# Optimization experiments

Hardware: AMD Instinct MI355X
Metric: run time of the kernel (lower is better)

The kernel has to match this reference:

```python
import jax
import jax.numpy as jnp
import numpy as np

NPOINT = 512
RADIUS = 0.2
K = 32


def setup_inputs() -> dict:
    key = jax.random.key(0)
    k1, k2 = jax.random.split(key)
    xyz = jax.random.uniform(k1, (8, 16384, 3), dtype=jnp.float32)      # [B,N,3] in unit cube
    features = jax.random.normal(k2, (8, 128, 16384), dtype=jnp.float32)  # [B,D,N]
    return {"xyz": xyz, "features": features}


def farthest_point_sample(xyz, npoint):
    # xyz: [B,N,3] -> centroids [B,npoint] int32. Deterministic start at index 0
    # (the torch code does randint(...)*0).
    B, N, _ = xyz.shape
    init_dist = jnp.full((B, N), 1e10, dtype=xyz.dtype)
    init_far = jnp.zeros((B,), dtype=jnp.int32)

    def step(carry, _):
        distance, farthest = carry
        centroid = jnp.take_along_axis(xyz, farthest[:, None, None], axis=1)  # [B,1,3]
        d = jnp.sum((xyz - centroid) ** 2, axis=-1)                           # [B,N]
        distance = jnp.minimum(distance, d)
        new_far = jnp.argmax(distance, axis=-1).astype(jnp.int32)
        return (distance, new_far), farthest

    (_, _), cents = jax.lax.scan(step, (init_dist, init_far), None, length=npoint)
    return cents.T  # [B, npoint]


def square_distance(src, dst):
    # src [B,S,3], dst [B,N,3] -> [B,S,N]
    d = -2.0 * jnp.einsum("bsc,bnc->bsn", src, dst)
    d = d + jnp.sum(src ** 2, -1)[:, :, None]
    d = d + jnp.sum(dst ** 2, -1)[:, None, :]
    return d


def query_ball_point(radius, nsample, xyz, new_xyz):
    B, N, _ = xyz.shape
    sqrd = square_distance(new_xyz, xyz)                              # [B,S,N]
    arangeN = jnp.arange(N, dtype=jnp.int32)[None, None, :]
    idx = jnp.where(sqrd > radius ** 2, N, arangeN)                   # out-of-ball -> sentinel N
    idx = jnp.sort(idx, axis=-1)[:, :, :nsample]                      # [B,S,K]
    first = idx[:, :, :1]
    idx = jnp.where(idx == N, first, idx)                             # pad with first valid neighbor
    return idx


def index_points(points, idx):
    # points [B,N,C], idx [B,...] -> [B,...,C]
    B = points.shape[0]
    bidx = jnp.arange(B).reshape((B,) + (1,) * (idx.ndim - 1))
    return points[bidx, idx]


def reference(xyz, features):
    # xyz [B,N,3], features [B,D,N]
    cent = farthest_point_sample(xyz, NPOINT)                 # [B,S]
    new_xyz = index_points(xyz, cent)                         # [B,S,3]
    idx = query_ball_point(RADIUS, K, xyz, new_xyz)           # [B,S,K]
    pts = jnp.transpose(features, (0, 2, 1))                  # [B,N,D]
    grouped = index_points(pts, idx)                          # [B,S,K,D]
    sub_features = jnp.max(grouped, axis=2)                   # [B,S,D]  (max over K neighbors)
    sub_features = jnp.transpose(sub_features, (0, 2, 1))     # [B,D,S]
    return new_xyz, sub_features
```

## Files before the change

kernel.cpp:

```cpp
#include <hip/hip_runtime.h>
#include <stdint.h>
#include <math.h>

#define NB      8
#define NPTS    16384
#define NPOINT  512
#define NCH     128
#define KNBR    32
#define R2      0.04f

#define FPS_THR 512
#define PPT     32

#define CENT_OFF 0
#define MAP_OFF  16384
#define FT_OFF   (16384 + 524288)

#define DPP_ARG_STEP(v, p, CTRL) do {                                          \
    float _ov = __builtin_bit_cast(float, __builtin_amdgcn_update_dpp(         \
        __builtin_bit_cast(int, (v)), __builtin_bit_cast(int, (v)),            \
        (CTRL), 0xF, 0xF, false));                                             \
    int _op = __builtin_amdgcn_update_dpp((p), (p), (CTRL), 0xF, 0xF, false);  \
    bool _t = (_ov > (v)) || ((_ov == (v)) && (_op < (p)));                    \
    (v) = _t ? _ov : (v);                                                      \
    (p) = _t ? _op : (p);                                                      \
} while (0)

__device__ __forceinline__ int cell_of(float x, float y, float z) {
    int cx = (int)(x * 8.0f); cx = cx < 0 ? 0 : (cx > 7 ? 7 : cx);
    int cy = (int)(y * 8.0f); cy = cy < 0 ? 0 : (cy > 7 ? 7 : cy);
    int cz = (int)(z * 8.0f); cz = cz < 0 ? 0 : (cz > 7 ? 7 : cz);
    int m = 0;
    m |= ((cx & 1) << 2) | ((cx & 2) << 4) | ((cx & 4) << 6);
    m |= ((cy & 1) << 1) | ((cy & 2) << 3) | ((cy & 4) << 5);
    m |=  (cz & 1)       | ((cz & 2) << 2) | ((cz & 4) << 4);
    return m;
}

__global__
__attribute__((amdgpu_flat_work_group_size(FPS_THR, FPS_THR)))
__attribute__((amdgpu_waves_per_eu(2, 2)))
void fps_transpose_kernel(const float* __restrict__ xyz,
                          const float* __restrict__ feat,
                          float* __restrict__ out,
                          int* __restrict__ cent,
                          int* __restrict__ map,
                          float* __restrict__ ft,
                          int use_ft)
{
    const int blk = blockIdx.x;
    const int tid = threadIdx.x;

    if (blk < NB) {
        const int b = blk;
        const float* xb = xyz + (size_t)b * NPTS * 3;
        int* gmap = map + b * NPTS;
        const int lane = tid & 63;
        const int wid  = tid >> 6;

        __shared__ int   s_hist[512];
        __shared__ float s_meta[8][PPT][4];
        __shared__ float s_v[2][8];
        __shared__ int   s_p[2][8];

        s_hist[tid] = 0;
        __syncthreads();
        for (int k = 0; k < PPT; ++k) {
            int p = k * FPS_THR + tid;
            int c = cell_of(xb[p * 3 + 0], xb[p * 3 + 1], xb[p * 3 + 2]);
            atomicAdd(&s_hist[c], 1);
        }
        __syncthreads();
        int mycount = s_hist[tid];
        for (int off = 1; off < 512; off <<= 1) {
            int v = (tid >= off) ? s_hist[tid - off] : 0;
            __syncthreads();
            s_hist[tid] += v;
            __syncthreads();
        }
        int excl = s_hist[tid] - mycount;
        __syncthreads();
        s_hist[tid] = excl;
        __syncthreads();
        for (int k = 0; k < PPT; ++k) {
            int p = k * FPS_THR + tid;
            int c = cell_of(xb[p * 3 + 0], xb[p * 3 + 1], xb[p * 3 + 2]);
            int pos = atomicAdd(&s_hist[c], 1);
            gmap[pos] = p;
        }
        __threadfence_block();
        __syncthreads();
        float px[PPT], py[PPT], pz[PPT], d[PPT];
        int   idx[PPT];
#pragma unroll
        for (int k = 0; k < PPT; ++k) {
            int pos = (k * 8 + wid) * 64 + lane;
            int op  = gmap[pos];
            idx[k] = op;
            px[k] = xb[op * 3 + 0];
            py[k] = xb[op * 3 + 1];
            pz[k] = xb[op * 3 + 2];
            d[k]  = 1e10f;
        }
#pragma unroll
        for (int k = 0; k < PPT; ++k) {
            float mnx = px[k], mxx = px[k];
            float mny = py[k], mxy = py[k];
            float mnz = pz[k], mxz = pz[k];
#pragma unroll
            for (int s = 1; s < 64; s <<= 1) {
                mnx = fminf(mnx, __shfl_xor(mnx, s, 64));
                mxx = fmaxf(mxx, __shfl_xor(mxx, s, 64));
                mny = fminf(mny, __shfl_xor(mny, s, 64));
                mxy = fmaxf(mxy, __shfl_xor(mxy, s, 64));
                mnz = fminf(mnz, __shfl_xor(mnz, s, 64));
                mxz = fmaxf(mxz, __shfl_xor(mxz, s, 64));
            }
            if (lane == 0) {
                float hx = (mxx - mnx) * 0.5f;
                float hy = (mxy - mny) * 0.5f;
                float hz = (mxz - mnz) * 0.5f;
                s_meta[wid][k][0] = (mnx + mxx) * 0.5f;
                s_meta[wid][k][1] = (mny + mxy) * 0.5f;
                s_meta[wid][k][2] = (mnz + mxz) * 0.5f;
                s_meta[wid][k][3] =
                    sqrtf(hx * hx + hy * hy + hz * hz) * 1.0001f + 1e-6f;
            }
        }
        __syncthreads();
        const float bmx = s_meta[wid][lane & 31][0];
        const float bmy = s_meta[wid][lane & 31][1];
        const float bmz = s_meta[wid][lane & 31][2];
        const float br  = s_meta[wid][lane & 31][3];
        float U = 1e10f;

        float cx = xb[0], cy = xb[1], cz = xb[2];
        if (tid == 0) {
            cent[b * NPOINT + 0] = 0;
            out[((size_t)b * NPOINT + 0) * 3 + 0] = cx;
            out[((size_t)b * NPOINT + 0) * 3 + 1] = cy;
            out[((size_t)b * NPOINT + 0) * 3 + 2] = cz;
        }

        for (int i = 1; i < NPOINT; ++i) {
            float dcx = cx - bmx, dcy = cy - bmy, dcz = cz - bmz;
            float dc  = sqrtf(dcx * dcx + dcy * dcy + dcz * dcz);
            float t   = dc - br;
            bool skip = (t > 0.0f) && (t * t >= U + 2e-5f);
            unsigned mask = (unsigned)__ballot(skip);

            if (mask != 0xFFFFFFFFu) {
#pragma unroll
                for (int k = 0; k < PPT; ++k) {
                    if (!(mask & (1u << k))) {
                        float dx = __fsub_rn(px[k], cx);
                        float dy = __fsub_rn(py[k], cy);
                        float dz = __fsub_rn(pz[k], cz);
                        float dd = __fadd_rn(__fadd_rn(__fmul_rn(dx, dx),
                                                       __fmul_rn(dy, dy)),
                                             __fmul_rn(dz, dz));
                        d[k] = fminf(d[k], dd);
                    }
                }
            }
            if (!((mask >> (lane & 31)) & 1u)) {
                float ub = dc + br;
                U = fminf(U, ub * ub * 1.0001f + 1e-6f);
            }
            float vmax = d[0];
#pragma unroll
            for (int k = 1; k < PPT; ++k) vmax = fmaxf(vmax, d[k]);
            int bi = idx[PPT - 1];
#pragma unroll
            for (int k = PPT - 2; k >= 0; --k) bi = (d[k] == vmax) ? idx[k] : bi;

            float rv = vmax;
            int   rp = bi;
            DPP_ARG_STEP(rv, rp, 0xB1);
            DPP_ARG_STEP(rv, rp, 0x4E);
            DPP_ARG_STEP(rv, rp, 0x141);
            DPP_ARG_STEP(rv, rp, 0x140);
            DPP_ARG_STEP(rv, rp, 0x142);
            DPP_ARG_STEP(rv, rp, 0x143);
            const int par = i & 1;
            if (lane == 63) { s_v[par][wid] = rv; s_p[par][wid] = rp; }
            __syncthreads();
            float fv = s_v[par][lane & 7];
            int   fp = s_p[par][lane & 7];
            DPP_ARG_STEP(fv, fp, 0xB1);
            DPP_ARG_STEP(fv, fp, 0x4E);
            DPP_ARG_STEP(fv, fp, 0x141);
            const int cur = __builtin_amdgcn_readfirstlane(fp);
            cx = xb[cur * 3 + 0];
            cy = xb[cur * 3 + 1];
            cz = xb[cur * 3 + 2];
            if (tid == 0) {
                cent[b * NPOINT + i] = cur;
                size_t o = ((size_t)b * NPOINT + i) * 3;
                out[o + 0] = cx; out[o + 1] = cy; out[o + 2] = cz;
            }
        }
    } else {
        if (!use_ft) return;
        int t  = blk - NB;
        int b  = t >> 11;
        int r  = t & 2047;
        int ct = r >> 9;
        int nt = r & 511;
        __shared__ float tile[32][33];
        int tx = tid & 31, ty = tid >> 5;
        tile[ty][tx] =
            feat[((size_t)b * NCH + ct * 32 + ty) * NPTS + nt * 32 + tx];
        tile[ty + 16][tx] =
            feat[((size_t)b * NCH + ct * 32 + ty + 16) * NPTS + nt * 32 + tx];
        __syncthreads();
        ft[((size_t)b * NPTS + nt * 32 + ty) * NCH + ct * 32 + tx] =
            tile[tx][ty];
        ft[((size_t)b * NPTS + nt * 32 + ty + 16) * NCH + ct * 32 + tx] =
            tile[tx][ty + 16];
    }
}

__global__ __launch_bounds__(256, 4)
void query_pool_kernel(const float* __restrict__ xyz,
                       const float* __restrict__ feat,
                       const float* __restrict__ ft,
                       const int* __restrict__ cent,
                       float* __restrict__ out_sub,
                       int use_ft)
{
    const int tid  = threadIdx.x;
    const int widx = tid >> 6;
    const int lane = tid & 63;
    const int w = blockIdx.x * 4 + widx;
    const int b = w >> 9;
    const int s = w & 511;

    const float* xb = xyz + (size_t)b * NPTS * 3;
    const int ci = cent[b * NPOINT + s];
    const float sx = xb[ci * 3 + 0];
    const float sy = xb[ci * 3 + 1];
    const float sz = xb[ci * 3 + 2];
    const float snorm = __fadd_rn(__fadd_rn(__fmul_rn(sx, sx),
                                            __fmul_rn(sy, sy)),
                                  __fmul_rn(sz, sz));

    __shared__ int lidx[4][KNBR];
    int found = 0;
    for (int base = 0; base < NPTS && found < KNBR; base += 64) {
        int j = base + lane;
        float dx = xb[j * 3 + 0];
        float dy = xb[j * 3 + 1];
        float dz = xb[j * 3 + 2];
        float dn = __fadd_rn(__fadd_rn(__fmul_rn(dx, dx),
                                       __fmul_rn(dy, dy)),
                             __fmul_rn(dz, dz));
        float dot = __fadd_rn(__fadd_rn(__fmul_rn(sx, dx),
                                        __fmul_rn(sy, dy)),
                              __fmul_rn(sz, dz));
        float d = __fadd_rn(__fadd_rn(__fmul_rn(-2.0f, dot), snorm), dn);
        bool inball = !(d > R2);
        unsigned long long mask = __ballot(inball);
        int before = (int)__popcll(mask & ((1ULL << lane) - 1ULL));
        int slot = found + before;
        if (inball && slot < KNBR) lidx[widx][slot] = j;
        found += (int)__popcll(mask);
    }
    int cnt = found < KNBR ? found : KNBR;
    __syncthreads();

    float a0 = -INFINITY, a1 = -INFINITY;
    if (use_ft) {
        for (int m = 0; m < cnt; ++m) {
            int i = lidx[widx][m];
            const float* row = ft + ((size_t)b * NPTS + i) * NCH;
            a0 = fmaxf(a0, row[lane]);
            a1 = fmaxf(a1, row[lane + 64]);
        }
    } else {
        for (int m = 0; m < cnt; ++m) {
            int i = lidx[widx][m];
            a0 = fmaxf(a0, feat[((size_t)b * NCH + lane) * NPTS + i]);
            a1 = fmaxf(a1, feat[((size_t)b * NCH + lane + 64) * NPTS + i]);
        }
    }
    out_sub[((size_t)b * NCH + lane) * NPOINT + s] = a0;
    out_sub[((size_t)b * NCH + lane + 64) * NPOINT + s] = a1;
}

extern "C" void kernel_launch(void* const* d_in, const int* in_sizes, int n_in,
                              void* d_out, int out_size, void* d_ws, size_t ws_size,
                              hipStream_t stream)
{
    const float* xyz  = (const float*)d_in[0];
    const float* feat = (const float*)d_in[1];
    float* out = (float*)d_out;

    int*   cent = (int*)((char*)d_ws + CENT_OFF);
    int*   map  = (int*)((char*)d_ws + MAP_OFF);
    float* ft   = (float*)((char*)d_ws + FT_OFF);
    const size_t need_ft = (size_t)FT_OFF + (size_t)NB * NPTS * NCH * 4ull;
    int use_ft = (ws_size >= need_ft) ? 1 : 0;

    int nblocks1 = NB + (use_ft ? NB * (NCH / 32) * (NPTS / 32) : 0);
    hipLaunchKernelGGL(fps_transpose_kernel, dim3(nblocks1), dim3(FPS_THR), 0, stream,
                       xyz, feat, out, cent, map, ft, use_ft);

    hipLaunchKernelGGL(query_pool_kernel, dim3((NB * NPOINT) / 4), dim3(256), 0, stream,
                       xyz, feat, ft, cent, out + (size_t)NB * NPOINT * 3, use_ft);
}
```

Baseline: 1.019 ms.

## Fuse FPS and ball-query pooling into one kernel with spin-wait on centroids

Measured after the change: 1.037 ms. About the same (+1.7%).

```diff
diff --git a/kernel.cpp b/kernel.cpp
--- a/kernel.cpp
+++ b/kernel.cpp
@@ -11,10 +11,10 @@
 
 #define FPS_THR 512
 #define PPT     32
+#define QBLKS   512
 
 #define CENT_OFF 0
 #define MAP_OFF  16384
-#define FT_OFF   (16384 + 524288)
 
 #define DPP_ARG_STEP(v, p, CTRL) do {                                          \
     float _ov = __builtin_bit_cast(float, __builtin_amdgcn_update_dpp(         \
@@ -39,24 +39,23 @@
 
 __global__
 __attribute__((amdgpu_flat_work_group_size(FPS_THR, FPS_THR)))
-__attribute__((amdgpu_waves_per_eu(2, 2)))
-void fps_transpose_kernel(const float* __restrict__ xyz,
-                          const float* __restrict__ feat,
-                          float* __restrict__ out,
-                          int* __restrict__ cent,
-                          int* __restrict__ map,
-                          float* __restrict__ ft,
-                          int use_ft)
+__attribute__((amdgpu_waves_per_eu(2, 4)))
+void fps_query_kernel(const float* __restrict__ xyz,
+                      const float* __restrict__ feat,
+                      float* __restrict__ out,
+                      int* __restrict__ cent,
+                      int* __restrict__ map,
+                      float* __restrict__ out_sub)
 {
     const int blk = blockIdx.x;
     const int tid = threadIdx.x;
+    const int lane = tid & 63;
+    const int wid  = tid >> 6;
 
     if (blk < NB) {
         const int b = blk;
         const float* xb = xyz + (size_t)b * NPTS * 3;
         int* gmap = map + b * NPTS;
-        const int lane = tid & 63;
-        const int wid  = tid >> 6;
 
         __shared__ int   s_hist[512];
         __shared__ float s_meta[8][PPT][4];
@@ -136,10 +135,11 @@
 
         float cx = xb[0], cy = xb[1], cz = xb[2];
         if (tid == 0) {
-            cent[b * NPOINT + 0] = 0;
             out[((size_t)b * NPOINT + 0) * 3 + 0] = cx;
             out[((size_t)b * NPOINT + 0) * 3 + 1] = cy;
             out[((size_t)b * NPOINT + 0) * 3 + 2] = cz;
+            __hip_atomic_store(&cent[b * NPOINT + 0], 0,
+                               __ATOMIC_RELAXED, __HIP_MEMORY_SCOPE_AGENT);
         }
 
         for (int i = 1; i < NPOINT; ++i) {
@@ -195,97 +195,66 @@
             cy = xb[cur * 3 + 1];
             cz = xb[cur * 3 + 2];
             if (tid == 0) {
-                cent[b * NPOINT + i] = cur;
                 size_t o = ((size_t)b * NPOINT + i) * 3;
                 out[o + 0] = cx; out[o + 1] = cy; out[o + 2] = cz;
+                __hip_atomic_store(&cent[b * NPOINT + i], cur,
+                                   __ATOMIC_RELAXED, __HIP_MEMORY_SCOPE_AGENT);
             }
         }
     } else {
-        if (!use_ft) return;
-        int t  = blk - NB;
-        int b  = t >> 11;
-        int r  = t & 2047;
-        int ct = r >> 9;
-        int nt = r & 511;
-        __shared__ float tile[32][33];
-        int tx = tid & 31, ty = tid >> 5;
-        tile[ty][tx] =
-            feat[((size_t)b * NCH + ct * 32 + ty) * NPTS + nt * 32 + tx];
-        tile[ty + 16][tx] =
-            feat[((size_t)b * NCH + ct * 32 + ty + 16) * NPTS + nt * 32 + tx];
-        __syncthreads();
-        ft[((size_t)b * NPTS + nt * 32 + ty) * NCH + ct * 32 + tx] =
-            tile[tx][ty];
-        ft[((size_t)b * NPTS + nt * 32 + ty + 16) * NCH + ct * 32 + tx] =
-            tile[tx][ty + 16];
+        __shared__ int lidx[8][KNBR];
+        const int wv = (blk - NB) * 8 + wid;
+        const int b  = wv >> 9;
+        const int s  = wv & 511;
+        const float* xb = xyz + (size_t)b * NPTS * 3;
+
+        int ci;
+        for (;;) {
+            ci = __hip_atomic_load(&cent[b * NPOINT + s],
+                                   __ATOMIC_RELAXED, __HIP_MEMORY_SCOPE_AGENT);
+            if (ci >= 0) break;
+            __builtin_amdgcn_s_sleep(8);
+        }
+
+        const float sx = xb[ci * 3 + 0];
+        const float sy = xb[ci * 3 + 1];
+        const float sz = xb[ci * 3 + 2];
+        const float snorm = __fadd_rn(__fadd_rn(__fmul_rn(sx, sx),
+                                                __fmul_rn(sy, sy)),
+                                      __fmul_rn(sz, sz));
+
+        int found = 0;
+        for (int base = 0; base < NPTS && found < KNBR; base += 64) {
+            int j = base + lane;
+            float dx = xb[j * 3 + 0];
+            float dy = xb[j * 3 + 1];
+            float dz = xb[j * 3 + 2];
+            float dn = __fadd_rn(__fadd_rn(__fmul_rn(dx, dx),
+                                           __fmul_rn(dy, dy)),
+                                 __fmul_rn(dz, dz));
+            float dot = __fadd_rn(__fadd_rn(__fmul_rn(sx, dx),
+                                            __fmul_rn(sy, dy)),
+                                  __fmul_rn(sz, dz));
+            float dqp = __fadd_rn(__fadd_rn(__fmul_rn(-2.0f, dot), snorm), dn);
+            bool inball = !(dqp > R2);
+            unsigned long long m = __ballot(inball);
+            int before = (int)__popcll(m & ((1ULL << lane) - 1ULL));
+            int slot = found + before;
+            if (inball && slot < KNBR) lidx[wid][slot] = j;
+            found += (int)__popcll(m);
+        }
+        int cnt = found < KNBR ? found : KNBR;
+
+        float a0 = -INFINITY, a1 = -INFINITY;
+        const float* fb = feat + (size_t)b * NCH * NPTS;
+        for (int m = 0; m < cnt; ++m) {
+            int i = lidx[wid][m];
+            a0 = fmaxf(a0, fb[(size_t)lane * NPTS + i]);
+            a1 = fmaxf(a1, fb[(size_t)(lane + 64) * NPTS + i]);
+        }
+        out_sub[((size_t)b * NCH + lane) * NPOINT + s] = a0;
+        out_sub[((size_t)b * NCH + lane + 64) * NPOINT + s] = a1;
     }
-}
-
-__global__ __launch_bounds__(256, 4)
-void query_pool_kernel(const float* __restrict__ xyz,
-                       const float* __restrict__ feat,
-                       const float* __restrict__ ft,
-                       const int* __restrict__ cent,
-                       float* __restrict__ out_sub,
-                       int use_ft)
-{
-    const int tid  = threadIdx.x;
-    const int widx = tid >> 6;
-    const int lane = tid & 63;
-    const int w = blockIdx.x * 4 + widx;
-    const int b = w >> 9;
-    const int s = w & 511;
-
-    const float* xb = xyz + (size_t)b * NPTS * 3;
-    const int ci = cent[b * NPOINT + s];
-    const float sx = xb[ci * 3 + 0];
-    const float sy = xb[ci * 3 + 1];
-    const float sz = xb[ci * 3 + 2];
-    const float snorm = __fadd_rn(__fadd_rn(__fmul_rn(sx, sx),
-                                            __fmul_rn(sy, sy)),
-                                  __fmul_rn(sz, sz));
-
-    __shared__ int lidx[4][KNBR];
-    int found = 0;
-    for (int base = 0; base < NPTS && found < KNBR; base += 64) {
-        int j = base + lane;
-        float dx = xb[j * 3 + 0];
-        float dy = xb[j * 3 + 1];
-        float dz = xb[j * 3 + 2];
-        float dn = __fadd_rn(__fadd_rn(__fmul_rn(dx, dx),
-                                       __fmul_rn(dy, dy)),
-                             __fmul_rn(dz, dz));
-        float dot = __fadd_rn(__fadd_rn(__fmul_rn(sx, dx),
-                                        __fmul_rn(sy, dy)),
-                              __fmul_rn(sz, dz));
-        float d = __fadd_rn(__fadd_rn(__fmul_rn(-2.0f, dot), snorm), dn);
-        bool inball = !(d > R2);
-        unsigned long long mask = __ballot(inball);
-        int before = (int)__popcll(mask & ((1ULL << lane) - 1ULL));
-        int slot = found + before;
-        if (inball && slot < KNBR) lidx[widx][slot] = j;
-        found += (int)__popcll(mask);
-    }
-    int cnt = found < KNBR ? found : KNBR;
-    __syncthreads();
-
-    float a0 = -INFINITY, a1 = -INFINITY;
-    if (use_ft) {
-        for (int m = 0; m < cnt; ++m) {
-            int i = lidx[widx][m];
-            const float* row = ft + ((size_t)b * NPTS + i) * NCH;
-            a0 = fmaxf(a0, row[lane]);
-            a1 = fmaxf(a1, row[lane + 64]);
-        }
-    } else {
-        for (int m = 0; m < cnt; ++m) {
-            int i = lidx[widx][m];
-            a0 = fmaxf(a0, feat[((size_t)b * NCH + lane) * NPTS + i]);
-            a1 = fmaxf(a1, feat[((size_t)b * NCH + lane + 64) * NPTS + i]);
-        }
-    }
-    out_sub[((size_t)b * NCH + lane) * NPOINT + s] = a0;
-    out_sub[((size_t)b * NCH + lane + 64) * NPOINT + s] = a1;
 }
 
 extern "C" void kernel_launch(void* const* d_in, const int* in_sizes, int n_in,
@@ -296,16 +265,12 @@
     const float* feat = (const float*)d_in[1];
     float* out = (float*)d_out;
 
-    int*   cent = (int*)((char*)d_ws + CENT_OFF);
-    int*   map  = (int*)((char*)d_ws + MAP_OFF);
-    float* ft   = (float*)((char*)d_ws + FT_OFF);
-    const size_t need_ft = (size_t)FT_OFF + (size_t)NB * NPTS * NCH * 4ull;
-    int use_ft = (ws_size >= need_ft) ? 1 : 0;
-
-    int nblocks1 = NB + (use_ft ? NB * (NCH / 32) * (NPTS / 32) : 0);
-    hipLaunchKernelGGL(fps_transpose_kernel, dim3(nblocks1), dim3(FPS_THR), 0, stream,
-                       xyz, feat, out, cent, map, ft, use_ft);
-
-    hipLaunchKernelGGL(query_pool_kernel, dim3((NB * NPOINT) / 4), dim3(256), 0, stream,
-                       xyz, feat, ft, cent, out + (size_t)NB * NPOINT * 3, use_ft);
+    int* cent = (int*)((char*)d_ws + CENT_OFF);
+    int* map  = (int*)((char*)d_ws + MAP_OFF);
+
+    hipMemsetAsync((char*)d_ws + CENT_OFF, 0xFF, NB * NPOINT * 4, stream);
+
+    hipLaunchKernelGGL(fps_query_kernel, dim3(NB + QBLKS), dim3(FPS_THR), 0,
+                       stream, xyz, feat, out, cent, map,
+                       out + (size_t)NB * NPOINT * 3);
 }
```
